# Optimization experiments

Measured on AMD Instinct MI355X. Metric: run time of the kernel, lower is better.

Reference implementation:

```python
import jax, jax.numpy as jnp
import numpy as np

NUM_USERS = 100000
NUM_ITEMS = 50000
NUM_BRANDS = 1000
N_NODES = NUM_USERS + NUM_ITEMS + NUM_BRANDS
EMBED_DIM = 64
N_LAYERS = 3
N_EDGES = 10000000


def setup_inputs() -> dict:
    key = jax.random.key(0)
    k1, k2, k3, k4, k5, k6 = jax.random.split(key, 6)
    adj_rows = jax.random.randint(k1, (N_EDGES,), 0, N_NODES, dtype=jnp.int64 if jax.config.jax_enable_x64 else jnp.int32)
    adj_cols = jax.random.randint(k2, (N_EDGES,), 0, N_NODES, dtype=jnp.int64 if jax.config.jax_enable_x64 else jnp.int32)
    adj_vals = jax.random.uniform(k3, (N_EDGES,), dtype=jnp.float32)
    user_emb = jax.random.normal(k4, (NUM_USERS, EMBED_DIM), dtype=jnp.float32)
    item_emb = jax.random.normal(k5, (NUM_ITEMS, EMBED_DIM), dtype=jnp.float32)
    brand_emb = jax.random.normal(k6, (NUM_BRANDS, EMBED_DIM), dtype=jnp.float32)
    return {
        "adj_rows": adj_rows,
        "adj_cols": adj_cols,
        "adj_vals": adj_vals,
        "user_emb": user_emb,
        "item_emb": item_emb,
        "brand_emb": brand_emb,
    }


def _spmm(rows, cols, vals, x, n_nodes):
    # y = A @ x for sparse COO A: gather source rows, scale, scatter-add to dest rows
    return jax.ops.segment_sum(vals[:, None] * x[cols], rows, num_segments=n_nodes)


def reference(adj_rows, adj_cols, adj_vals, user_emb, item_emb, brand_emb):
    n_users = user_emb.shape[0]
    n_items = item_emb.shape[0]
    n_nodes = n_users + n_items + brand_emb.shape[0]
    ego = jnp.concatenate([user_emb, item_emb, brand_emb], axis=0)  # [N, D]
    acc = ego  # running sum over layers (fused stack+mean)
    for _ in range(N_LAYERS):
        ego = _spmm(adj_rows, adj_cols, adj_vals, ego, n_nodes)
        acc = acc + ego
    final = acc / jnp.asarray(N_LAYERS + 1, dtype=acc.dtype)
    final_user = final[:n_users]
    final_item = final[n_users:n_users + n_items]
    final_brand = final[n_users + n_items:]
    return (final_user, final_item, final_brand, user_emb, item_emb)
```

## Files before the change

### kernel.cpp

```cpp
#include <hip/hip_runtime.h>
#include <hip/hip_bf16.h>
#include <stdint.h>

#define NU 100000
#define NI 50000
#define NB 1000
#define NN 151000
#define D  64
#define NE 10000000

#define BSH   6
#define BROWS 64
#define NBUCK 2360
#define CAPB  5632
#define BINB  512
#define BINT  1024
#define PSTR  2368

typedef unsigned short u16;
typedef unsigned int   u32;

__device__ __forceinline__ u16 f2bf(float f) {
    union { float f; u32 i; } c; c.f = f;
    u32 lsb = (c.i >> 16) & 1;
    c.i += 0x7fffu + lsb;
    return (u16)(c.i >> 16);
}

__global__ __launch_bounds__(BINT) void k_bin(
    const int* __restrict__ rows, const int* __restrict__ cols,
    const float* __restrict__ vals,
    int* __restrict__ prefarr, int2* __restrict__ subbuf) {
    __shared__ int hcnt[NBUCK];
    __shared__ int hcur[NBUCK];
    __shared__ int tsum[BINT];
    int b = blockIdx.x, tid = threadIdx.x;
    long e0 = (long)b * NE / BINB;
    long e1 = (long)(b + 1) * NE / BINB;
    for (int j = tid; j < NBUCK; j += BINT) hcnt[j] = 0;
    __syncthreads();
    for (long i = e0 + tid; i < e1; i += BINT)
        atomicAdd(&hcnt[rows[i] >> BSH], 1);
    __syncthreads();
    int base3 = tid * 3;
    int v0 = (base3     < NBUCK) ? hcnt[base3]     : 0;
    int v1 = (base3 + 1 < NBUCK) ? hcnt[base3 + 1] : 0;
    int v2 = (base3 + 2 < NBUCK) ? hcnt[base3 + 2] : 0;
    int lsum = v0 + v1 + v2;
    tsum[tid] = lsum;
    __syncthreads();
    for (int d = 1; d < BINT; d <<= 1) {
        int t = (tid >= d) ? tsum[tid - d] : 0;
        __syncthreads();
        tsum[tid] += t;
        __syncthreads();
    }
    int excl = tsum[tid] - lsum;
    int* prow = prefarr + (size_t)b * PSTR;
    if (base3     < NBUCK) { hcur[base3]     = excl;           prow[base3]     = excl; }
    if (base3 + 1 < NBUCK) { hcur[base3 + 1] = excl + v0;      prow[base3 + 1] = excl + v0; }
    if (base3 + 2 < NBUCK) { hcur[base3 + 2] = excl + v0 + v1; prow[base3 + 2] = excl + v0 + v1; }
    if (tid == BINT - 1) prow[NBUCK] = tsum[tid];
    __syncthreads();
    for (long i = e0 + tid; i < e1; i += BINT) {
        int r  = rows[i];
        int bk = r >> BSH;
        int pos = atomicAdd(&hcur[bk], 1);
        subbuf[e0 + pos] =
            make_int2(((r & (BROWS - 1)) << 18) | cols[i], __float_as_int(vals[i]));
    }
}

__global__ __launch_bounds__(256) void k_csr(
    const int* __restrict__ prefarr, const int2* __restrict__ subbuf,
    int* __restrict__ off, int* __restrict__ cnt, int* __restrict__ gtotal,
    int2* __restrict__ cicv) {
    __shared__ int rcnt[BROWS], rexc[BROWS], lcur[BROWS];
    __shared__ int csta[BINB], clen[BINB];
    __shared__ int sbase, stot;
    __shared__ int2 sbuf[CAPB];
    int b = blockIdx.x, tid = threadIdx.x;
    for (int blk = tid; blk < BINB; blk += 256) {
        const int* prow = prefarr + (size_t)blk * PSTR;
        int s = prow[b];
        int e = prow[b + 1];
        csta[blk] = (int)((long)blk * NE / BINB) + s;
        clen[blk] = e - s;
    }
    if (tid < BROWS) rcnt[tid] = 0;
    __syncthreads();
    for (int blk = tid; blk < BINB; blk += 256) {
        const int2* src = subbuf + csta[blk];
        int l = clen[blk];
        for (int k = 0; k < l; ++k)
            atomicAdd(&rcnt[(u32)src[k].x >> 18], 1);
    }
    __syncthreads();
    if (tid < 64) {
        int v = rcnt[tid], x = v;
        for (int d = 1; d < 64; d <<= 1) {
            int t = __shfl_up(x, d);
            if (tid >= d) x += t;
        }
        rexc[tid] = x - v;
        if (tid == 63) {
            stot = x;
            sbase = atomicAdd(gtotal, x);
        }
    }
    __syncthreads();
    int base = sbase;
    if (tid < BROWS) {
        int r = b * BROWS + tid;
        if (r < NN) { off[r] = base + rexc[tid]; cnt[r] = rcnt[tid]; }
        lcur[tid] = rexc[tid];
    }
    __syncthreads();
    for (int blk = tid; blk < BINB; blk += 256) {
        const int2* src = subbuf + csta[blk];
        int l = clen[blk];
        for (int k = 0; k < l; ++k) {
            int2 rec = src[k];
            int rl = (u32)rec.x >> 18;
            int dst = atomicAdd(&lcur[rl], 1);
            if (dst < CAPB) sbuf[dst] = make_int2(rec.x & 0x3FFFF, rec.y);
        }
    }
    __syncthreads();
    int T = stot; if (T > CAPB) T = CAPB;
    for (int j = tid; j < T; j += 256)
        cicv[base + j] = sbuf[j];
}

__global__ void k_init(const float4* __restrict__ ue, const float4* __restrict__ ie,
                       const float4* __restrict__ be, ushort4* __restrict__ xa,
                       float4* __restrict__ acc, float4* __restrict__ out4) {
    int i4 = blockIdx.x * blockDim.x + threadIdx.x;
    if (i4 >= NN * D / 4) return;
    float4 v;
    if (i4 < NU * D / 4)             v = ue[i4];
    else if (i4 < (NU + NI) * D / 4) v = ie[i4 - NU * D / 4];
    else                             v = be[i4 - (NU + NI) * D / 4];
    acc[i4] = v;
    ushort4 h;
    h.x = f2bf(v.x); h.y = f2bf(v.y); h.z = f2bf(v.z); h.w = f2bf(v.w);
    xa[i4] = h;
    if (i4 < (NU + NI) * D / 4)
        out4[NN * D / 4 + i4] = v;
}

__device__ __forceinline__ void acc8(float f, uint4 h, float* s) {
    union { u32 i; float v; } t;
    t.i = h.x << 16;         s[0] += f * t.v;
    t.i = h.x & 0xffff0000u; s[1] += f * t.v;
    t.i = h.y << 16;         s[2] += f * t.v;
    t.i = h.y & 0xffff0000u; s[3] += f * t.v;
    t.i = h.z << 16;         s[4] += f * t.v;
    t.i = h.z & 0xffff0000u; s[5] += f * t.v;
    t.i = h.w << 16;         s[6] += f * t.v;
    t.i = h.w & 0xffff0000u; s[7] += f * t.v;
}

template<int LAST>
__global__ __launch_bounds__(256) void k_spmm(
    const int* __restrict__ off, const int* __restrict__ cnt,
    const int2* __restrict__ cicv,
    const u16* __restrict__ xin, uint4* __restrict__ xout,
    float4* __restrict__ acc, float4* __restrict__ out) {
    int gid  = blockIdx.x * blockDim.x + threadIdx.x;
    int row  = gid >> 6;
    int lane = threadIdx.x & 63;
    if (row >= NN) return;
    int base = __builtin_amdgcn_readfirstlane(off[row]);
    int deg  = __builtin_amdgcn_readfirstlane(cnt[row]);
    int q = lane >> 3;
    int p = lane & 7;
    float s[8] = {0.f, 0.f, 0.f, 0.f, 0.f, 0.f, 0.f, 0.f};
    for (int e = 0; e < deg; e += 32) {
        int2 r0 = cicv[base + e + q];
        int2 r1 = cicv[base + e + 8 + q];
        int2 r2 = cicv[base + e + 16 + q];
        int2 r3 = cicv[base + e + 24 + q];
        bool ok0 = (e + q)      < deg;
        bool ok1 = (e + 8 + q)  < deg;
        bool ok2 = (e + 16 + q) < deg;
        bool ok3 = (e + 24 + q) < deg;
        int c0 = ok0 ? r0.x : 0;  float f0 = ok0 ? __int_as_float(r0.y) : 0.f;
        int c1 = ok1 ? r1.x : 0;  float f1 = ok1 ? __int_as_float(r1.y) : 0.f;
        int c2 = ok2 ? r2.x : 0;  float f2 = ok2 ? __int_as_float(r2.y) : 0.f;
        int c3 = ok3 ? r3.x : 0;  float f3 = ok3 ? __int_as_float(r3.y) : 0.f;
        uint4 h0 = *(const uint4*)(xin + (size_t)c0 * D + p * 8);
        uint4 h1 = *(const uint4*)(xin + (size_t)c1 * D + p * 8);
        uint4 h2 = *(const uint4*)(xin + (size_t)c2 * D + p * 8);
        uint4 h3 = *(const uint4*)(xin + (size_t)c3 * D + p * 8);
        acc8(f0, h0, s);
        acc8(f1, h1, s);
        acc8(f2, h2, s);
        acc8(f3, h3, s);
    }
#pragma unroll
    for (int k = 0; k < 8; ++k) {
        s[k] += __shfl_xor(s[k], 8);
        s[k] += __shfl_xor(s[k], 16);
        s[k] += __shfl_xor(s[k], 32);
    }
    int o16 = row * 16 + p * 2;
    if (LAST) {
        if (q == 0) {
            float4 a0 = acc[o16], a1 = acc[o16 + 1];
            out[o16]     = make_float4((a0.x + s[0]) * 0.25f, (a0.y + s[1]) * 0.25f,
                                       (a0.z + s[2]) * 0.25f, (a0.w + s[3]) * 0.25f);
            out[o16 + 1] = make_float4((a1.x + s[4]) * 0.25f, (a1.y + s[5]) * 0.25f,
                                       (a1.z + s[6]) * 0.25f, (a1.w + s[7]) * 0.25f);
        }
    } else {
        if (q == 0) {
            float4 a0 = acc[o16], a1 = acc[o16 + 1];
            acc[o16]     = make_float4(a0.x + s[0], a0.y + s[1], a0.z + s[2], a0.w + s[3]);
            acc[o16 + 1] = make_float4(a1.x + s[4], a1.y + s[5], a1.z + s[6], a1.w + s[7]);
        } else if (q == 1) {
            uint4 hh;
            hh.x = (u32)f2bf(s[0]) | ((u32)f2bf(s[1]) << 16);
            hh.y = (u32)f2bf(s[2]) | ((u32)f2bf(s[3]) << 16);
            hh.z = (u32)f2bf(s[4]) | ((u32)f2bf(s[5]) << 16);
            hh.w = (u32)f2bf(s[6]) | ((u32)f2bf(s[7]) << 16);
            xout[row * 8 + p] = hh;
        }
    }
}

extern "C" void kernel_launch(void* const* d_in, const int* in_sizes, int n_in,
                              void* d_out, int out_size, void* d_ws, size_t ws_size,
                              hipStream_t stream) {
    const int*   rows = (const int*)d_in[0];
    const int*   cols = (const int*)d_in[1];
    const float* vals = (const float*)d_in[2];
    float* out = (float*)d_out;

    char* w = (char*)d_ws;
    size_t p = 0;
#define WALLOC(var, type, count) \
    type* var = (type*)(w + p); p += (((size_t)(count) * sizeof(type)) + 255) & ~(size_t)255;
    WALLOC(gtotal,  int, 64)
    WALLOC(off,     int, NN)
    WALLOC(cnt,     int, NN)
    WALLOC(prefarr, int, (size_t)BINB * PSTR)
    size_t regA = p;
    int2* subbuf = (int2*)(w + regA);
    size_t subbuf_sz = ((size_t)NE * sizeof(int2) + 255) & ~(size_t)255;
    u16*   xa  = (u16*)(w + regA);
    u16*   xb  = (u16*)(w + regA + (size_t)NN * D * sizeof(u16));
    float* acc = (float*)(w + regA + 2 * (size_t)NN * D * sizeof(u16));
    p = regA + subbuf_sz;
    WALLOC(cicv, int2, (size_t)NE + 32)
#undef WALLOC
    (void)p; (void)ws_size; (void)in_sizes; (void)n_in; (void)out_size;

    hipMemsetAsync(gtotal, 0, sizeof(int), stream);

    k_bin<<<BINB, BINT, 0, stream>>>(rows, cols, vals, prefarr, subbuf);
    k_csr<<<NBUCK, 256, 0, stream>>>(prefarr, subbuf, off, cnt, gtotal, cicv);
    k_init<<<(NN * D / 4 + 255) / 256, 256, 0, stream>>>(
        (const float4*)d_in[3], (const float4*)d_in[4],
        (const float4*)d_in[5], (ushort4*)xa, (float4*)acc, (float4*)out);

    int spmm_blocks = NN / 4;
    k_spmm<0><<<spmm_blocks, 256, 0, stream>>>(off, cnt, cicv, xa, (uint4*)xb,
                                               (float4*)acc, (float4*)out);
    k_spmm<0><<<spmm_blocks, 256, 0, stream>>>(off, cnt, cicv, xb, (uint4*)xa,
                                               (float4*)acc, (float4*)out);
    k_spmm<1><<<spmm_blocks, 256, 0, stream>>>(off, cnt, cicv, xa, (uint4*)xb,
                                               (float4*)acc, (float4*)out);
}
```

Before: 1.034 ms.

## Stage binning in LDS, drop fp32 accumulator, unroll SpMM gather to 64 edges

k_bin now scatters records into an LDS buffer and then writes them out to global memory in one coalesced pass, with three times as many blocks. The fp32 running accumulator is removed: each layer is kept in bf16, and the last SpMM sums x0, y1, y2 and its own result to form the mean. The SpMM inner loop processes 64 edges per iteration with 8 independent gathers to expose more memory-level parallelism. The aims are less scattered global write traffic and no per-layer fp32 acc read-modify-write. In exchange, the final sum now uses bf16-rounded copies of the original and intermediate embeddings, which lowers precision, and k_csr has to merge more, smaller segments.

Measured after the change: 936.0 us. 1.11x faster.

```diff
diff --git a/kernel.cpp b/kernel.cpp
--- a/kernel.cpp
+++ b/kernel.cpp
@@ -13,8 +13,9 @@
 #define BROWS 64
 #define NBUCK 2360
 #define CAPB  5632
-#define BINB  512
+#define BINB  1536
 #define BINT  1024
+#define SBCAP 6512
 #define PSTR  2368
 
 typedef unsigned short u16;
@@ -27,25 +28,37 @@
     return (u16)(c.i >> 16);
 }
 
+__device__ __forceinline__ void cvt8(uint4 h, float* f) {
+    union { u32 i; float v; } t;
+    t.i = h.x << 16;         f[0] = t.v;
+    t.i = h.x & 0xffff0000u; f[1] = t.v;
+    t.i = h.y << 16;         f[2] = t.v;
+    t.i = h.y & 0xffff0000u; f[3] = t.v;
+    t.i = h.z << 16;         f[4] = t.v;
+    t.i = h.z & 0xffff0000u; f[5] = t.v;
+    t.i = h.w << 16;         f[6] = t.v;
+    t.i = h.w & 0xffff0000u; f[7] = t.v;
+}
+
 __global__ __launch_bounds__(BINT) void k_bin(
     const int* __restrict__ rows, const int* __restrict__ cols,
     const float* __restrict__ vals,
     int* __restrict__ prefarr, int2* __restrict__ subbuf) {
-    __shared__ int hcnt[NBUCK];
-    __shared__ int hcur[NBUCK];
-    __shared__ int tsum[BINT];
+    __shared__ int hc[NBUCK];
+    __shared__ int2 sbuf[SBCAP];
+    int* tsum = (int*)sbuf;
     int b = blockIdx.x, tid = threadIdx.x;
     long e0 = (long)b * NE / BINB;
     long e1 = (long)(b + 1) * NE / BINB;
-    for (int j = tid; j < NBUCK; j += BINT) hcnt[j] = 0;
+    for (int j = tid; j < NBUCK; j += BINT) hc[j] = 0;
     __syncthreads();
     for (long i = e0 + tid; i < e1; i += BINT)
-        atomicAdd(&hcnt[rows[i] >> BSH], 1);
+        atomicAdd(&hc[rows[i] >> BSH], 1);
     __syncthreads();
     int base3 = tid * 3;
-    int v0 = (base3     < NBUCK) ? hcnt[base3]     : 0;
-    int v1 = (base3 + 1 < NBUCK) ? hcnt[base3 + 1] : 0;
-    int v2 = (base3 + 2 < NBUCK) ? hcnt[base3 + 2] : 0;
+    int v0 = (base3     < NBUCK) ? hc[base3]     : 0;
+    int v1 = (base3 + 1 < NBUCK) ? hc[base3 + 1] : 0;
+    int v2 = (base3 + 2 < NBUCK) ? hc[base3 + 2] : 0;
     int lsum = v0 + v1 + v2;
     tsum[tid] = lsum;
     __syncthreads();
@@ -57,18 +70,21 @@
     }
     int excl = tsum[tid] - lsum;
     int* prow = prefarr + (size_t)b * PSTR;
-    if (base3     < NBUCK) { hcur[base3]     = excl;           prow[base3]     = excl; }
-    if (base3 + 1 < NBUCK) { hcur[base3 + 1] = excl + v0;      prow[base3 + 1] = excl + v0; }
-    if (base3 + 2 < NBUCK) { hcur[base3 + 2] = excl + v0 + v1; prow[base3 + 2] = excl + v0 + v1; }
+    if (base3     < NBUCK) { hc[base3]     = excl;           prow[base3]     = excl; }
+    if (base3 + 1 < NBUCK) { hc[base3 + 1] = excl + v0;      prow[base3 + 1] = excl + v0; }
+    if (base3 + 2 < NBUCK) { hc[base3 + 2] = excl + v0 + v1; prow[base3 + 2] = excl + v0 + v1; }
     if (tid == BINT - 1) prow[NBUCK] = tsum[tid];
     __syncthreads();
     for (long i = e0 + tid; i < e1; i += BINT) {
-        int r  = rows[i];
-        int bk = r >> BSH;
-        int pos = atomicAdd(&hcur[bk], 1);
-        subbuf[e0 + pos] =
-            make_int2(((r & (BROWS - 1)) << 18) | cols[i], __float_as_int(vals[i]));
-    }
+        int r = rows[i];
+        int pos = atomicAdd(&hc[r >> BSH], 1);
+        sbuf[pos] = make_int2(((r & (BROWS - 1)) << 18) | cols[i],
+                              __float_as_int(vals[i]));
+    }
+    __syncthreads();
+    int T = (int)(e1 - e0);
+    for (int j = tid; j < T; j += BINT)
+        subbuf[e0 + j] = sbuf[j];
 }
 
 __global__ __launch_bounds__(256) void k_csr(
@@ -133,32 +149,26 @@
 }
 
 __global__ void k_init(const float4* __restrict__ ue, const float4* __restrict__ ie,
-                       const float4* __restrict__ be, ushort4* __restrict__ xa,
-                       float4* __restrict__ acc, float4* __restrict__ out4) {
+                       const float4* __restrict__ be, ushort4* __restrict__ x0,
+                       float4* __restrict__ out4) {
     int i4 = blockIdx.x * blockDim.x + threadIdx.x;
     if (i4 >= NN * D / 4) return;
     float4 v;
     if (i4 < NU * D / 4)             v = ue[i4];
     else if (i4 < (NU + NI) * D / 4) v = ie[i4 - NU * D / 4];
     else                             v = be[i4 - (NU + NI) * D / 4];
-    acc[i4] = v;
     ushort4 h;
     h.x = f2bf(v.x); h.y = f2bf(v.y); h.z = f2bf(v.z); h.w = f2bf(v.w);
-    xa[i4] = h;
+    x0[i4] = h;
     if (i4 < (NU + NI) * D / 4)
         out4[NN * D / 4 + i4] = v;
 }
 
 __device__ __forceinline__ void acc8(float f, uint4 h, float* s) {
-    union { u32 i; float v; } t;
-    t.i = h.x << 16;         s[0] += f * t.v;
-    t.i = h.x & 0xffff0000u; s[1] += f * t.v;
-    t.i = h.y << 16;         s[2] += f * t.v;
-    t.i = h.y & 0xffff0000u; s[3] += f * t.v;
-    t.i = h.z << 16;         s[4] += f * t.v;
-    t.i = h.z & 0xffff0000u; s[5] += f * t.v;
-    t.i = h.w << 16;         s[6] += f * t.v;
-    t.i = h.w & 0xffff0000u; s[7] += f * t.v;
+    float x[8];
+    cvt8(h, x);
+#pragma unroll
+    for (int k = 0; k < 8; ++k) s[k] += f * x[k];
 }
 
 template<int LAST>
@@ -166,7 +176,8 @@
     const int* __restrict__ off, const int* __restrict__ cnt,
     const int2* __restrict__ cicv,
     const u16* __restrict__ xin, uint4* __restrict__ xout,
-    float4* __restrict__ acc, float4* __restrict__ out) {
+    const u16* __restrict__ b0, const u16* __restrict__ b1,
+    float4* __restrict__ out) {
     int gid  = blockIdx.x * blockDim.x + threadIdx.x;
     int row  = gid >> 6;
     int lane = threadIdx.x & 63;
@@ -176,27 +187,26 @@
     int q = lane >> 3;
     int p = lane & 7;
     float s[8] = {0.f, 0.f, 0.f, 0.f, 0.f, 0.f, 0.f, 0.f};
-    for (int e = 0; e < deg; e += 32) {
-        int2 r0 = cicv[base + e + q];
-        int2 r1 = cicv[base + e + 8 + q];
-        int2 r2 = cicv[base + e + 16 + q];
-        int2 r3 = cicv[base + e + 24 + q];
-        bool ok0 = (e + q)      < deg;
-        bool ok1 = (e + 8 + q)  < deg;
-        bool ok2 = (e + 16 + q) < deg;
-        bool ok3 = (e + 24 + q) < deg;
-        int c0 = ok0 ? r0.x : 0;  float f0 = ok0 ? __int_as_float(r0.y) : 0.f;
-        int c1 = ok1 ? r1.x : 0;  float f1 = ok1 ? __int_as_float(r1.y) : 0.f;
-        int c2 = ok2 ? r2.x : 0;  float f2 = ok2 ? __int_as_float(r2.y) : 0.f;
-        int c3 = ok3 ? r3.x : 0;  float f3 = ok3 ? __int_as_float(r3.y) : 0.f;
-        uint4 h0 = *(const uint4*)(xin + (size_t)c0 * D + p * 8);
-        uint4 h1 = *(const uint4*)(xin + (size_t)c1 * D + p * 8);
-        uint4 h2 = *(const uint4*)(xin + (size_t)c2 * D + p * 8);
-        uint4 h3 = *(const uint4*)(xin + (size_t)c3 * D + p * 8);
-        acc8(f0, h0, s);
-        acc8(f1, h1, s);
-        acc8(f2, h2, s);
-        acc8(f3, h3, s);
+    for (int e = 0; e < deg; e += 64) {
+        int2 rr[8];
+#pragma unroll
+        for (int k = 0; k < 8; ++k)
+            rr[k] = cicv[base + e + 8 * k + q];
+        int   c[8];
+        float f[8];
+#pragma unroll
+        for (int k = 0; k < 8; ++k) {
+            bool ok = (e + 8 * k + q) < deg;
+            c[k] = ok ? rr[k].x : 0;
+            f[k] = ok ? __int_as_float(rr[k].y) : 0.f;
+        }
+        uint4 h[8];
+#pragma unroll
+        for (int k = 0; k < 8; ++k)
+            h[k] = *(const uint4*)(xin + (size_t)c[k] * D + p * 8);
+#pragma unroll
+        for (int k = 0; k < 8; ++k)
+            acc8(f[k], h[k], s);
     }
 #pragma unroll
     for (int k = 0; k < 8; ++k) {
@@ -204,21 +214,25 @@
         s[k] += __shfl_xor(s[k], 16);
         s[k] += __shfl_xor(s[k], 32);
     }
-    int o16 = row * 16 + p * 2;
     if (LAST) {
         if (q == 0) {
-            float4 a0 = acc[o16], a1 = acc[o16 + 1];
-            out[o16]     = make_float4((a0.x + s[0]) * 0.25f, (a0.y + s[1]) * 0.25f,
-                                       (a0.z + s[2]) * 0.25f, (a0.w + s[3]) * 0.25f);
-            out[o16 + 1] = make_float4((a1.x + s[4]) * 0.25f, (a1.y + s[5]) * 0.25f,
-                                       (a1.z + s[6]) * 0.25f, (a1.w + s[7]) * 0.25f);
+            uint4 h0 = *(const uint4*)(b0  + (size_t)row * D + p * 8);
+            uint4 h1 = *(const uint4*)(b1  + (size_t)row * D + p * 8);
+            uint4 h2 = *(const uint4*)(xin + (size_t)row * D + p * 8);
+            float f0[8], f1[8], f2[8];
+            cvt8(h0, f0); cvt8(h1, f1); cvt8(h2, f2);
+            int o16 = row * 16 + p * 2;
+            out[o16]     = make_float4((f0[0]+f1[0]+f2[0]+s[0])*0.25f,
+                                       (f0[1]+f1[1]+f2[1]+s[1])*0.25f,
+                                       (f0[2]+f1[2]+f2[2]+s[2])*0.25f,
+                                       (f0[3]+f1[3]+f2[3]+s[3])*0.25f);
+            out[o16 + 1] = make_float4((f0[4]+f1[4]+f2[4]+s[4])*0.25f,
+                                       (f0[5]+f1[5]+f2[5]+s[5])*0.25f,
+                                       (f0[6]+f1[6]+f2[6]+s[6])*0.25f,
+                                       (f0[7]+f1[7]+f2[7]+s[7])*0.25f);
         }
     } else {
         if (q == 0) {
-            float4 a0 = acc[o16], a1 = acc[o16 + 1];
-            acc[o16]     = make_float4(a0.x + s[0], a0.y + s[1], a0.z + s[2], a0.w + s[3]);
-            acc[o16 + 1] = make_float4(a1.x + s[4], a1.y + s[5], a1.z + s[6], a1.w + s[7]);
-        } else if (q == 1) {
             uint4 hh;
             hh.x = (u32)f2bf(s[0]) | ((u32)f2bf(s[1]) << 16);
             hh.y = (u32)f2bf(s[2]) | ((u32)f2bf(s[3]) << 16);
@@ -248,11 +262,11 @@
     size_t regA = p;
     int2* subbuf = (int2*)(w + regA);
     size_t subbuf_sz = ((size_t)NE * sizeof(int2) + 255) & ~(size_t)255;
-    u16*   xa  = (u16*)(w + regA);
-    u16*   xb  = (u16*)(w + regA + (size_t)NN * D * sizeof(u16));
-    float* acc = (float*)(w + regA + 2 * (size_t)NN * D * sizeof(u16));
+    u16* x0 = (u16*)(w + regA);
+    u16* y1 = (u16*)(w + regA + (size_t)NN * D * sizeof(u16));
+    u16* y2 = (u16*)(w + regA + 2 * (size_t)NN * D * sizeof(u16));
     p = regA + subbuf_sz;
-    WALLOC(cicv, int2, (size_t)NE + 32)
+    WALLOC(cicv, int2, (size_t)NE + 64)
 #undef WALLOC
     (void)p; (void)ws_size; (void)in_sizes; (void)n_in; (void)out_size;
 
@@ -262,13 +276,13 @@
     k_csr<<<NBUCK, 256, 0, stream>>>(prefarr, subbuf, off, cnt, gtotal, cicv);
     k_init<<<(NN * D / 4 + 255) / 256, 256, 0, stream>>>(
         (const float4*)d_in[3], (const float4*)d_in[4],
-        (const float4*)d_in[5], (ushort4*)xa, (float4*)acc, (float4*)out);
+        (const float4*)d_in[5], (ushort4*)x0, (float4*)out);
 
     int spmm_blocks = NN / 4;
-    k_spmm<0><<<spmm_blocks, 256, 0, stream>>>(off, cnt, cicv, xa, (uint4*)xb,
-                                               (float4*)acc, (float4*)out);
-    k_spmm<0><<<spmm_blocks, 256, 0, stream>>>(off, cnt, cicv, xb, (uint4*)xa,
-                                               (float4*)acc, (float4*)out);
-    k_spmm<1><<<spmm_blocks, 256, 0, stream>>>(off, cnt, cicv, xa, (uint4*)xb,
-                                               (float4*)acc, (float4*)out);
-}
+    k_spmm<0><<<spmm_blocks, 256, 0, stream>>>(off, cnt, cicv, x0, (uint4*)y1,
+                                               x0, x0, (float4*)out);
+    k_spmm<0><<<spmm_blocks, 256, 0, stream>>>(off, cnt, cicv, y1, (uint4*)y2,
+                                               x0, x0, (float4*)out);
+    k_spmm<1><<<spmm_blocks, 256, 0, stream>>>(off, cnt, cicv, y2, (uint4*)y1,
+                                               x0, y1, (float4*)out);
+}
```
